# Optimization experiments

Measured on AMD Instinct MI355X. Metric: run time of the kernel, lower is better.

## Reference

```python
import jax, jax.numpy as jnp
import numpy as np

B, C, H, W = 8, 512, 64, 32
SE_MID = C // 16
BN_EPS = 1e-5


def conv1x1(x, w, b):
    # x: [B,Cin,H,W], w: [Cout,Cin], b: [Cout]
    return jnp.einsum('bchw,oc->bohw', x, w) + b[None, :, None, None]


def setup_inputs() -> dict:
    key = jax.random.key(0)
    ks = jax.random.split(key, 17)
    s = 0.05
    return {
        'x': jax.random.normal(ks[0], (B, C, H, W), jnp.float32),
        'g_w': jax.random.normal(ks[1], (1, C), jnp.float32) * s,
        'g_b': jax.random.normal(ks[2], (1,), jnp.float32) * s,
        'theta_w': jax.random.normal(ks[3], (1, C), jnp.float32) * s,
        'theta_b': jax.random.normal(ks[4], (1,), jnp.float32) * s,
        'phi_w': jax.random.normal(ks[5], (1, C), jnp.float32) * s,
        'phi_b': jax.random.normal(ks[6], (1,), jnp.float32) * s,
        'W_w': jax.random.normal(ks[7], (C, 1), jnp.float32) * s,
        'W_b': jax.random.normal(ks[8], (C,), jnp.float32) * s,
        'bn_gamma': jax.random.normal(ks[9], (C,), jnp.float32) * s + 1.0,
        'bn_beta': jax.random.normal(ks[10], (C,), jnp.float32) * s,
        'bn_mean': jax.random.normal(ks[11], (C,), jnp.float32) * s,
        'bn_var': jax.random.uniform(ks[12], (C,), jnp.float32, 0.5, 1.5),
        'se1_w': jax.random.normal(ks[13], (SE_MID, C), jnp.float32) * s,
        'se1_b': jnp.zeros((SE_MID,), jnp.float32),
        'se2_w': jax.random.normal(ks[14], (C, SE_MID), jnp.float32) * s,
        'se2_b': jnp.zeros((C,), jnp.float32),
    }


def reference(x, g_w, g_b, theta_w, theta_b, phi_w, phi_b, W_w, W_b,
              bn_gamma, bn_beta, bn_mean, bn_var, se1_w, se1_b, se2_w, se2_b):
    b, c, h, w = x.shape
    N = h * w
    # SE channel gate from global average pool: [B,C,1,1]
    x_avg = jnp.mean(x, axis=(2, 3), keepdims=True)
    se_mid = jax.nn.relu(conv1x1(x_avg, se1_w, se1_b))
    W_cw = jax.nn.sigmoid(conv1x1(se_mid, se2_w, se2_b))  # [B,C,1,1]

    # inter_channels == 1: each projection is a length-N vector per sample
    g_x = conv1x1(x, g_w, g_b).reshape(b, N)          # [B,N]
    theta_x = conv1x1(x, theta_w, theta_b).reshape(b, N)  # [B,N]
    phi_x = conv1x1(x, phi_w, phi_b).reshape(b, N)        # [B,N]

    # f[b,i,j] = theta[b,i] * phi[b,j]; row softmax over j; y = f_div_C @ g
    f = theta_x[:, :, None] * phi_x[:, None, :]       # [B,N,N]
    f_div_C = jax.nn.softmax(f, axis=-1)
    y = jnp.einsum('bij,bj->bi', f_div_C, g_x)        # [B,N]
    y = y.reshape(b, 1, h, w)

    # W: 1x1 conv (1 -> C) + BatchNorm2d (inference form with running stats)
    W_y = conv1x1(y, W_w, W_b)                        # [B,C,H,W]
    inv = bn_gamma / jnp.sqrt(bn_var + BN_EPS)
    W_y = (W_y - bn_mean[None, :, None, None]) * inv[None, :, None, None] \
          + bn_beta[None, :, None, None]

    return W_cw * W_y + x
```

## Files before the change

kernel.cpp:

```cpp
#include <hip/hip_runtime.h>

#define BB 8
#define CC 512
#define NN 2048
#define SEM 32
#define BN_EPS 1e-5f

#define NCC 16
#define NCHUNK (CC / NCC)
#define PIX 1024

__global__ __launch_bounds__(256) void k1(const float* __restrict__ x,
    const float* __restrict__ gw, const float* __restrict__ tw, const float* __restrict__ pw,
    float* __restrict__ pp,
    float* __restrict__ avgp)
{
    int tid = threadIdx.x;
    int wave = tid >> 6, lane = tid & 63;
    int blk = blockIdx.x;
    int ic = blk & 1;
    int cc = (blk >> 1) & (NCHUNK - 1);
    int b  = blk >> 6;
    int c0 = cc * NCC;

    const float4* xp = reinterpret_cast<const float4*>(x)
                     + ((size_t)(b * CC + c0) * (NN / 4)) + ic * (PIX / 4);

    float4 ag = {0,0,0,0}, at_ = {0,0,0,0}, ap = {0,0,0,0};
    float s[NCC];

    #pragma unroll
    for (int c = 0; c < NCC; ++c) {
        float4 v = xp[(size_t)c * (NN / 4) + tid];
        float wgc = gw[c0 + c], wtc = tw[c0 + c], wpc = pw[c0 + c];
        ag.x = fmaf(wgc, v.x, ag.x); ag.y = fmaf(wgc, v.y, ag.y);
        ag.z = fmaf(wgc, v.z, ag.z); ag.w = fmaf(wgc, v.w, ag.w);
        at_.x = fmaf(wtc, v.x, at_.x); at_.y = fmaf(wtc, v.y, at_.y);
        at_.z = fmaf(wtc, v.z, at_.z); at_.w = fmaf(wtc, v.w, at_.w);
        ap.x = fmaf(wpc, v.x, ap.x); ap.y = fmaf(wpc, v.y, ap.y);
        ap.z = fmaf(wpc, v.z, ap.z); ap.w = fmaf(wpc, v.w, ap.w);
        s[c] = (v.x + v.y) + (v.z + v.w);
    }

    size_t base = (((size_t)b * 2 + ic) * NCHUNK + cc) * PIX + tid * 4;
    const size_t karr = (size_t)BB * 2 * NCHUNK * PIX;
    *reinterpret_cast<float4*>(pp + 0 * karr + base) = ag;
    *reinterpret_cast<float4*>(pp + 1 * karr + base) = at_;
    *reinterpret_cast<float4*>(pp + 2 * karr + base) = ap;

    #pragma unroll
    for (int o = 32; o > 0; o >>= 1) {
        #pragma unroll
        for (int c = 0; c < NCC; ++c)
            s[c] += __shfl_down(s[c], o);
    }
    if (lane == 0) {
        #pragma unroll
        for (int c = 0; c < NCC; ++c)
            avgp[(size_t)(b * CC + c0 + c) * 8 + ic * 4 + wave] = s[c];
    }
}

__global__ __launch_bounds__(256) void k2(
    const float* __restrict__ pp,
    const float* __restrict__ gb, const float* __restrict__ tb, const float* __restrict__ pb,
    float* __restrict__ gx, float* __restrict__ tx, float* __restrict__ px)
{
    int tid = threadIdx.x;
    int half = blockIdx.x & 1;
    int ic   = (blockIdx.x >> 1) & 1;
    int b    = blockIdx.x >> 2;
    int p    = half * 512 + tid * 2;
    size_t base = ((((size_t)b * 2 + ic) * NCHUNK) * PIX + p) / 2;
    const size_t karr2 = (size_t)BB * 2 * NCHUNK * PIX / 2;
    const float2* pp2 = reinterpret_cast<const float2*>(pp);
    float2 g = {0,0}, t = {0,0}, ph = {0,0};
    #pragma unroll 8
    for (int cc = 0; cc < NCHUNK; ++cc) {
        float2 a = pp2[0 * karr2 + base + cc * (PIX / 2)];
        float2 c = pp2[1 * karr2 + base + cc * (PIX / 2)];
        float2 d = pp2[2 * karr2 + base + cc * (PIX / 2)];
        g.x += a.x;  g.y += a.y;
        t.x += c.x;  t.y += c.y;
        ph.x += d.x; ph.y += d.y;
    }
    int o = b * NN + ic * PIX + p;
    float gbv = gb[0], tbv = tb[0], pbv = pb[0];
    *reinterpret_cast<float2*>(gx + o) = make_float2(g.x + gbv, g.y + gbv);
    *reinterpret_cast<float2*>(tx + o) = make_float2(t.x + tbv, t.y + tbv);
    *reinterpret_cast<float2*>(px + o) = make_float2(ph.x + pbv, ph.y + pbv);
}

__global__ __launch_bounds__(256) void k3(
    const float* __restrict__ gx, const float* __restrict__ tx,
    const float* __restrict__ px, const float* __restrict__ avgp,
    const float* __restrict__ se1w, const float* __restrict__ se1b,
    const float* __restrict__ se2w, const float* __restrict__ se2b,
    const float* __restrict__ Ww, const float* __restrict__ Wb,
    const float* __restrict__ gamma, const float* __restrict__ beta,
    const float* __restrict__ mean, const float* __restrict__ var,
    float* __restrict__ y, float* __restrict__ Ac, float* __restrict__ Dc)
{
    int tid = threadIdx.x;

    if (blockIdx.x >= 1024) {
        int b = blockIdx.x - 1024;
        __shared__ float sA[CC];
        __shared__ float sP[SEM][8];
        __shared__ float sM[SEM];
        for (int c = tid; c < CC; c += 256) {
            const float* apt = avgp + (size_t)(b * CC + c) * 8;
            float s = 0.f;
            #pragma unroll
            for (int k = 0; k < 8; ++k) s += apt[k];
            sA[c] = s * (1.0f / NN);
        }
        __syncthreads();
        {
            int m = tid >> 3, sub = tid & 7;
            const float* w1 = se1w + m * CC + sub * 64;
            const float* a1 = sA + sub * 64;
            float s = 0.f;
            #pragma unroll
            for (int k = 0; k < 64; ++k) s = fmaf(a1[k], w1[k], s);
            sP[m][sub] = s;
        }
        __syncthreads();
        if (tid < SEM) {
            float t = 0.f;
            #pragma unroll
            for (int k = 0; k < 8; ++k) t += sP[tid][k];
            sM[tid] = fmaxf(t + se1b[tid], 0.f);
        }
        __syncthreads();
        for (int c = tid; c < CC; c += 256) {
            float s2 = 0.f;
            #pragma unroll
            for (int m = 0; m < SEM; ++m) s2 = fmaf(sM[m], se2w[c * SEM + m], s2);
            s2 += se2b[c];
            float wcw = 1.f / (1.f + __expf(-s2));
            float inv = gamma[c] * rsqrtf(var[c] + BN_EPS);
            Ac[b * CC + c] = wcw * Ww[c] * inv;
            Dc[b * CC + c] = wcw * ((Wb[c] - mean[c]) * inv + beta[c]);
        }
        return;
    }

    __shared__ float2 pg[NN];
    int b  = blockIdx.x >> 7;
    int i0 = (blockIdx.x & 127) << 4;
    for (int j = tid; j < NN; j += 256)
        pg[j] = make_float2(px[b * NN + j], gx[b * NN + j]);
    __syncthreads();

    int wave = tid >> 6, lane = tid & 63;
    int r0 = i0 + wave * 4;
    float t0 = tx[b * NN + r0 + 0];
    float t1 = tx[b * NN + r0 + 1];
    float t2 = tx[b * NN + r0 + 2];
    float t3 = tx[b * NN + r0 + 3];
    float s0 = 0.f, g0 = 0.f, s1 = 0.f, g1 = 0.f;
    float s2 = 0.f, g2 = 0.f, s3 = 0.f, g3 = 0.f;
    #pragma unroll 4
    for (int j = lane; j < NN; j += 64) {
        float2 v = pg[j];
        float e0 = __expf(fminf(t0 * v.x, 80.f));
        float e1 = __expf(fminf(t1 * v.x, 80.f));
        float e2 = __expf(fminf(t2 * v.x, 80.f));
        float e3 = __expf(fminf(t3 * v.x, 80.f));
        s0 += e0; g0 = fmaf(e0, v.y, g0);
        s1 += e1; g1 = fmaf(e1, v.y, g1);
        s2 += e2; g2 = fmaf(e2, v.y, g2);
        s3 += e3; g3 = fmaf(e3, v.y, g3);
    }
    for (int o = 32; o > 0; o >>= 1) {
        s0 += __shfl_down(s0, o); g0 += __shfl_down(g0, o);
        s1 += __shfl_down(s1, o); g1 += __shfl_down(g1, o);
        s2 += __shfl_down(s2, o); g2 += __shfl_down(g2, o);
        s3 += __shfl_down(s3, o); g3 += __shfl_down(g3, o);
    }
    if (lane == 0) {
        y[b * NN + r0 + 0] = g0 / s0;
        y[b * NN + r0 + 1] = g1 / s1;
        y[b * NN + r0 + 2] = g2 / s2;
        y[b * NN + r0 + 3] = g3 / s3;
    }
}

__global__ __launch_bounds__(256) void k4(
    const float* __restrict__ x, const float* __restrict__ y,
    const float* __restrict__ Ac, const float* __restrict__ Dc,
    float* __restrict__ out)
{
    int bc = blockIdx.x;
    int b = bc >> 9;
    float a = Ac[bc], d = Dc[bc];
    const float4* x4 = reinterpret_cast<const float4*>(x) + (size_t)bc * (NN / 4);
    const float4* y4 = reinterpret_cast<const float4*>(y) + (size_t)b * (NN / 4);
    float4* o4 = reinterpret_cast<float4*>(out) + (size_t)bc * (NN / 4);
    int tid = threadIdx.x;
    #pragma unroll
    for (int k = 0; k < 2; ++k) {
        int idx = k * 256 + tid;
        float4 xv = x4[idx], yv = y4[idx], ov;
        ov.x = fmaf(a, yv.x, d) + xv.x;
        ov.y = fmaf(a, yv.y, d) + xv.y;
        ov.z = fmaf(a, yv.z, d) + xv.z;
        ov.w = fmaf(a, yv.w, d) + xv.w;
        o4[idx] = ov;
    }
}

extern "C" void kernel_launch(void* const* d_in, const int* in_sizes, int n_in,
                              void* d_out, int out_size, void* d_ws, size_t ws_size,
                              hipStream_t stream) {
    const float* x    = (const float*)d_in[0];
    const float* gw   = (const float*)d_in[1];
    const float* gb   = (const float*)d_in[2];
    const float* tw   = (const float*)d_in[3];
    const float* tb   = (const float*)d_in[4];
    const float* pw   = (const float*)d_in[5];
    const float* pb   = (const float*)d_in[6];
    const float* Ww   = (const float*)d_in[7];
    const float* Wb   = (const float*)d_in[8];
    const float* gam  = (const float*)d_in[9];
    const float* bet  = (const float*)d_in[10];
    const float* mu   = (const float*)d_in[11];
    const float* var  = (const float*)d_in[12];
    const float* se1w = (const float*)d_in[13];
    const float* se1b = (const float*)d_in[14];
    const float* se2w = (const float*)d_in[15];
    const float* se2b = (const float*)d_in[16];

    float* ws   = (float*)d_ws;
    float* pp   = ws; ws += 3 * BB * 2 * NCHUNK * PIX;
    float* avgp = ws; ws += BB * CC * 8;
    float* gx   = ws; ws += BB * NN;
    float* tx   = ws; ws += BB * NN;
    float* px   = ws; ws += BB * NN;
    float* y    = ws; ws += BB * NN;
    float* Ac   = ws; ws += BB * CC;
    float* Dc   = ws; ws += BB * CC;
    float* out  = (float*)d_out;

    k1<<<BB * NCHUNK * 2, 256, 0, stream>>>(x, gw, tw, pw, pp, avgp);
    k2<<<BB * 2 * 2, 256, 0, stream>>>(pp, gb, tb, pb, gx, tx, px);
    k3<<<1024 + BB, 256, 0, stream>>>(gx, tx, px, avgp, se1w, se1b, se2w, se2b,
                                      Ww, Wb, gam, bet, mu, var, y, Ac, Dc);
    k4<<<BB * CC, 256, 0, stream>>>(x, y, Ac, Dc, out);
}
```

Baseline: 39.19 us.

## Fuse four kernels into one cooperative kernel with grid-wide syncs

Replaces the four separate launches with a single cooperative kernel of 256 blocks × 1024 threads, separated by grid.sync() between phases, with a multi-launch fallback if the cooperative launch fails. It also reshapes the per-phase work (full-row chunks in phase 1, 1024-thread reductions in phase 2, 16 channel rows per block in phase 4) and folds the g bias into Dc. The aim is to remove launch gaps and tail effects between the small kernels. In exchange it adds grid barrier cost and occupies only 256 blocks, which may underuse the GPU in the memory-bound phases.

After: 133.0 us. 3.39x slower.

```diff
diff --git a/kernel.cpp b/kernel.cpp
--- a/kernel.cpp
+++ b/kernel.cpp
@@ -1,164 +1,149 @@
 #include <hip/hip_runtime.h>
+#include <hip/hip_cooperative_groups.h>
+
+namespace cg = cooperative_groups;
 
 #define BB 8
 #define CC 512
 #define NN 2048
 #define SEM 32
 #define BN_EPS 1e-5f
-
 #define NCC 16
-#define NCHUNK (CC / NCC)
-#define PIX 1024
-
-__global__ __launch_bounds__(256) void k1(const float* __restrict__ x,
-    const float* __restrict__ gw, const float* __restrict__ tw, const float* __restrict__ pw,
-    float* __restrict__ pp,
-    float* __restrict__ avgp)
-{
-    int tid = threadIdx.x;
-    int wave = tid >> 6, lane = tid & 63;
-    int blk = blockIdx.x;
-    int ic = blk & 1;
-    int cc = (blk >> 1) & (NCHUNK - 1);
-    int b  = blk >> 6;
-    int c0 = cc * NCC;
-
-    const float4* xp = reinterpret_cast<const float4*>(x)
-                     + ((size_t)(b * CC + c0) * (NN / 4)) + ic * (PIX / 4);
-
-    float4 ag = {0,0,0,0}, at_ = {0,0,0,0}, ap = {0,0,0,0};
+#define NCHUNK 32
+#define KARR (BB * NCHUNK * NN)
+
+struct Ptrs {
+    const float *x, *gw, *tw, *pw, *gb, *tb, *pb;
+    const float *se1w, *se1b, *se2w, *se2b, *Ww, *Wb, *gam, *bet, *mu, *var;
+    float *pp, *avgp, *gx, *tx, *px, *y, *Ac, *Dc, *out;
+};
+
+__device__ __forceinline__ void phase1(const Ptrs& p, int blk, int tid) {
+    int b = blk >> 5, cc = blk & 31, c0 = cc * NCC;
+    const float2* xp2 = reinterpret_cast<const float2*>(p.x)
+                      + (size_t)(b * CC + c0) * (NN / 2) + tid;
+    float2 v[NCC];
+    #pragma unroll
+    for (int c = 0; c < NCC; ++c) v[c] = xp2[c * (NN / 2)];
+
+    float2 ag = {0,0}, at_ = {0,0}, ap = {0,0};
     float s[NCC];
-
     #pragma unroll
     for (int c = 0; c < NCC; ++c) {
-        float4 v = xp[(size_t)c * (NN / 4) + tid];
-        float wgc = gw[c0 + c], wtc = tw[c0 + c], wpc = pw[c0 + c];
-        ag.x = fmaf(wgc, v.x, ag.x); ag.y = fmaf(wgc, v.y, ag.y);
-        ag.z = fmaf(wgc, v.z, ag.z); ag.w = fmaf(wgc, v.w, ag.w);
-        at_.x = fmaf(wtc, v.x, at_.x); at_.y = fmaf(wtc, v.y, at_.y);
-        at_.z = fmaf(wtc, v.z, at_.z); at_.w = fmaf(wtc, v.w, at_.w);
-        ap.x = fmaf(wpc, v.x, ap.x); ap.y = fmaf(wpc, v.y, ap.y);
-        ap.z = fmaf(wpc, v.z, ap.z); ap.w = fmaf(wpc, v.w, ap.w);
-        s[c] = (v.x + v.y) + (v.z + v.w);
-    }
-
-    size_t base = (((size_t)b * 2 + ic) * NCHUNK + cc) * PIX + tid * 4;
-    const size_t karr = (size_t)BB * 2 * NCHUNK * PIX;
-    *reinterpret_cast<float4*>(pp + 0 * karr + base) = ag;
-    *reinterpret_cast<float4*>(pp + 1 * karr + base) = at_;
-    *reinterpret_cast<float4*>(pp + 2 * karr + base) = ap;
+        float wg = p.gw[c0 + c], wt = p.tw[c0 + c], wp = p.pw[c0 + c];
+        ag.x  = fmaf(wg, v[c].x, ag.x);  ag.y  = fmaf(wg, v[c].y, ag.y);
+        at_.x = fmaf(wt, v[c].x, at_.x); at_.y = fmaf(wt, v[c].y, at_.y);
+        ap.x  = fmaf(wp, v[c].x, ap.x);  ap.y  = fmaf(wp, v[c].y, ap.y);
+        s[c] = v[c].x + v[c].y;
+    }
+
+    size_t base = (size_t)blk * (NN / 2) + tid;
+    reinterpret_cast<float2*>(p.pp)[base] = ag;
+    reinterpret_cast<float2*>(p.pp + KARR)[base] = at_;
+    reinterpret_cast<float2*>(p.pp + 2 * (size_t)KARR)[base] = ap;
 
     #pragma unroll
     for (int o = 32; o > 0; o >>= 1) {
         #pragma unroll
-        for (int c = 0; c < NCC; ++c)
-            s[c] += __shfl_down(s[c], o);
-    }
+        for (int c = 0; c < NCC; ++c) s[c] += __shfl_down(s[c], o);
+    }
+    int wave = tid >> 6, lane = tid & 63;
     if (lane == 0) {
         #pragma unroll
         for (int c = 0; c < NCC; ++c)
-            avgp[(size_t)(b * CC + c0 + c) * 8 + ic * 4 + wave] = s[c];
-    }
-}
-
-__global__ __launch_bounds__(256) void k2(
-    const float* __restrict__ pp,
-    const float* __restrict__ gb, const float* __restrict__ tb, const float* __restrict__ pb,
-    float* __restrict__ gx, float* __restrict__ tx, float* __restrict__ px)
-{
-    int tid = threadIdx.x;
-    int half = blockIdx.x & 1;
-    int ic   = (blockIdx.x >> 1) & 1;
-    int b    = blockIdx.x >> 2;
-    int p    = half * 512 + tid * 2;
-    size_t base = ((((size_t)b * 2 + ic) * NCHUNK) * PIX + p) / 2;
-    const size_t karr2 = (size_t)BB * 2 * NCHUNK * PIX / 2;
-    const float2* pp2 = reinterpret_cast<const float2*>(pp);
-    float2 g = {0,0}, t = {0,0}, ph = {0,0};
-    #pragma unroll 8
-    for (int cc = 0; cc < NCHUNK; ++cc) {
-        float2 a = pp2[0 * karr2 + base + cc * (PIX / 2)];
-        float2 c = pp2[1 * karr2 + base + cc * (PIX / 2)];
-        float2 d = pp2[2 * karr2 + base + cc * (PIX / 2)];
-        g.x += a.x;  g.y += a.y;
-        t.x += c.x;  t.y += c.y;
-        ph.x += d.x; ph.y += d.y;
-    }
-    int o = b * NN + ic * PIX + p;
-    float gbv = gb[0], tbv = tb[0], pbv = pb[0];
-    *reinterpret_cast<float2*>(gx + o) = make_float2(g.x + gbv, g.y + gbv);
-    *reinterpret_cast<float2*>(tx + o) = make_float2(t.x + tbv, t.y + tbv);
-    *reinterpret_cast<float2*>(px + o) = make_float2(ph.x + pbv, ph.y + pbv);
-}
-
-__global__ __launch_bounds__(256) void k3(
-    const float* __restrict__ gx, const float* __restrict__ tx,
-    const float* __restrict__ px, const float* __restrict__ avgp,
-    const float* __restrict__ se1w, const float* __restrict__ se1b,
-    const float* __restrict__ se2w, const float* __restrict__ se2b,
-    const float* __restrict__ Ww, const float* __restrict__ Wb,
-    const float* __restrict__ gamma, const float* __restrict__ beta,
-    const float* __restrict__ mean, const float* __restrict__ var,
-    float* __restrict__ y, float* __restrict__ Ac, float* __restrict__ Dc)
-{
-    int tid = threadIdx.x;
-
-    if (blockIdx.x >= 1024) {
-        int b = blockIdx.x - 1024;
-        __shared__ float sA[CC];
-        __shared__ float sP[SEM][8];
-        __shared__ float sM[SEM];
-        for (int c = tid; c < CC; c += 256) {
-            const float* apt = avgp + (size_t)(b * CC + c) * 8;
-            float s = 0.f;
-            #pragma unroll
-            for (int k = 0; k < 8; ++k) s += apt[k];
-            sA[c] = s * (1.0f / NN);
-        }
-        __syncthreads();
-        {
-            int m = tid >> 3, sub = tid & 7;
-            const float* w1 = se1w + m * CC + sub * 64;
-            const float* a1 = sA + sub * 64;
-            float s = 0.f;
-            #pragma unroll
-            for (int k = 0; k < 64; ++k) s = fmaf(a1[k], w1[k], s);
-            sP[m][sub] = s;
+            p.avgp[(size_t)(b * CC + c0 + c) * 16 + wave] = s[c];
+    }
+}
+
+__device__ __forceinline__ void phase2(const Ptrs& p, int blk, int tid, float* smem) {
+    if (blk < 64) {
+        int b = blk >> 3, oct = blk & 7;
+        int pxi = tid & 255, rep = tid >> 8;
+        int pix = oct * 256 + pxi;
+        const float* base0 = p.pp + (size_t)b * NCHUNK * NN + pix + (size_t)rep * 8 * NN;
+        float a0 = 0.f, a1 = 0.f, a2 = 0.f;
+        #pragma unroll
+        for (int c = 0; c < 8; ++c) {
+            a0 += base0[(size_t)c * NN];
+            a1 += base0[(size_t)c * NN + KARR];
+            a2 += base0[(size_t)c * NN + 2 * (size_t)KARR];
+        }
+        smem[rep * 256 + pxi]        = a0;
+        smem[1024 + rep * 256 + pxi] = a1;
+        smem[2048 + rep * 256 + pxi] = a2;
+        __syncthreads();
+        if (tid < 768) {
+            int k = tid >> 8, px2 = tid & 255;
+            float* sk = smem + k * 1024;
+            float v = sk[px2] + sk[256 + px2] + sk[512 + px2] + sk[768 + px2];
+            int o = b * NN + oct * 256 + px2;
+            if (k == 0)      p.gx[o] = v;
+            else if (k == 1) p.tx[o] = v + p.tb[0];
+            else             p.px[o] = v + p.pb[0];
+        }
+    } else if (blk < 72) {
+        int b = blk - 64;
+        float* sA = smem;
+        float* sP = smem + 512;
+        float* sM = smem + 1024;
+        if (tid < 512) {
+            const float* apt = p.avgp + (size_t)(b * CC + tid) * 16;
+            float ssum = 0.f;
+            #pragma unroll
+            for (int k = 0; k < 16; ++k) ssum += apt[k];
+            sA[tid] = ssum * (1.0f / NN);
+        }
+        __syncthreads();
+        if (tid < 512) {
+            int m = tid >> 4, sub = tid & 15;
+            const float* w1 = p.se1w + m * CC + sub * 32;
+            const float* a1 = sA + sub * 32;
+            float ssum = 0.f;
+            #pragma unroll
+            for (int k = 0; k < 32; ++k) ssum = fmaf(a1[k], w1[k], ssum);
+            sP[m * 16 + sub] = ssum;
         }
         __syncthreads();
         if (tid < SEM) {
             float t = 0.f;
             #pragma unroll
-            for (int k = 0; k < 8; ++k) t += sP[tid][k];
-            sM[tid] = fmaxf(t + se1b[tid], 0.f);
-        }
-        __syncthreads();
-        for (int c = tid; c < CC; c += 256) {
+            for (int k = 0; k < 16; ++k) t += sP[tid * 16 + k];
+            sM[tid] = fmaxf(t + p.se1b[tid], 0.f);
+        }
+        __syncthreads();
+        if (tid < 512) {
+            int c = tid;
             float s2 = 0.f;
             #pragma unroll
-            for (int m = 0; m < SEM; ++m) s2 = fmaf(sM[m], se2w[c * SEM + m], s2);
-            s2 += se2b[c];
+            for (int m = 0; m < SEM; ++m) s2 = fmaf(sM[m], p.se2w[c * SEM + m], s2);
+            s2 += p.se2b[c];
             float wcw = 1.f / (1.f + __expf(-s2));
-            float inv = gamma[c] * rsqrtf(var[c] + BN_EPS);
-            Ac[b * CC + c] = wcw * Ww[c] * inv;
-            Dc[b * CC + c] = wcw * ((Wb[c] - mean[c]) * inv + beta[c]);
-        }
-        return;
-    }
-
-    __shared__ float2 pg[NN];
-    int b  = blockIdx.x >> 7;
-    int i0 = (blockIdx.x & 127) << 4;
-    for (int j = tid; j < NN; j += 256)
-        pg[j] = make_float2(px[b * NN + j], gx[b * NN + j]);
+            float inv = p.gam[c] * rsqrtf(p.var[c] + BN_EPS);
+            float A = wcw * p.Ww[c] * inv;
+            p.Ac[b * CC + c] = A;
+            p.Dc[b * CC + c] = wcw * ((p.Wb[c] - p.mu[c]) * inv + p.bet[c]) + A * p.gb[0];
+        }
+    }
+}
+
+__device__ __forceinline__ void phase3(const Ptrs& p, int blk, int tid, float* smem) {
+    float2* pg = reinterpret_cast<float2*>(smem);
+    int b = blk >> 5, rg = blk & 31;
+    const float* pxr = p.px + b * NN;
+    const float* gxr = p.gx + b * NN;
+    #pragma unroll
+    for (int j0 = 0; j0 < 2; ++j0) {
+        int j = j0 * 1024 + tid;
+        pg[j] = make_float2(pxr[j], gxr[j]);
+    }
     __syncthreads();
 
     int wave = tid >> 6, lane = tid & 63;
-    int r0 = i0 + wave * 4;
-    float t0 = tx[b * NN + r0 + 0];
-    float t1 = tx[b * NN + r0 + 1];
-    float t2 = tx[b * NN + r0 + 2];
-    float t3 = tx[b * NN + r0 + 3];
+    int r0 = rg * 64 + wave * 4;
+    float t0 = p.tx[b * NN + r0 + 0];
+    float t1 = p.tx[b * NN + r0 + 1];
+    float t2 = p.tx[b * NN + r0 + 2];
+    float t3 = p.tx[b * NN + r0 + 3];
     float s0 = 0.f, g0 = 0.f, s1 = 0.f, g1 = 0.f;
     float s2 = 0.f, g2 = 0.f, s3 = 0.f, g3 = 0.f;
     #pragma unroll 4
@@ -180,72 +165,104 @@
         s3 += __shfl_down(s3, o); g3 += __shfl_down(g3, o);
     }
     if (lane == 0) {
-        y[b * NN + r0 + 0] = g0 / s0;
-        y[b * NN + r0 + 1] = g1 / s1;
-        y[b * NN + r0 + 2] = g2 / s2;
-        y[b * NN + r0 + 3] = g3 / s3;
-    }
-}
-
-__global__ __launch_bounds__(256) void k4(
-    const float* __restrict__ x, const float* __restrict__ y,
-    const float* __restrict__ Ac, const float* __restrict__ Dc,
-    float* __restrict__ out)
-{
-    int bc = blockIdx.x;
-    int b = bc >> 9;
-    float a = Ac[bc], d = Dc[bc];
-    const float4* x4 = reinterpret_cast<const float4*>(x) + (size_t)bc * (NN / 4);
-    const float4* y4 = reinterpret_cast<const float4*>(y) + (size_t)b * (NN / 4);
-    float4* o4 = reinterpret_cast<float4*>(out) + (size_t)bc * (NN / 4);
-    int tid = threadIdx.x;
-    #pragma unroll
-    for (int k = 0; k < 2; ++k) {
-        int idx = k * 256 + tid;
-        float4 xv = x4[idx], yv = y4[idx], ov;
-        ov.x = fmaf(a, yv.x, d) + xv.x;
-        ov.y = fmaf(a, yv.y, d) + xv.y;
-        ov.z = fmaf(a, yv.z, d) + xv.z;
-        ov.w = fmaf(a, yv.w, d) + xv.w;
-        o4[idx] = ov;
-    }
-}
+        p.y[b * NN + r0 + 0] = g0 / s0;
+        p.y[b * NN + r0 + 1] = g1 / s1;
+        p.y[b * NN + r0 + 2] = g2 / s2;
+        p.y[b * NN + r0 + 3] = g3 / s3;
+    }
+}
+
+__device__ __forceinline__ void phase4(const Ptrs& p, int blk, int tid) {
+    int bc0 = blk * 16;
+    int b = blk >> 5;
+    int f4 = tid & 511, rr = tid >> 9;
+    float4 yv = reinterpret_cast<const float4*>(p.y + (size_t)b * NN)[f4];
+    float av[8], dv[8];
+    float4 xv[8];
+    #pragma unroll
+    for (int r = 0; r < 8; ++r) {
+        int bc = bc0 + rr * 8 + r;
+        av[r] = p.Ac[bc];
+        dv[r] = p.Dc[bc];
+        xv[r] = reinterpret_cast<const float4*>(p.x)[(size_t)bc * (NN / 4) + f4];
+    }
+    #pragma unroll
+    for (int r = 0; r < 8; ++r) {
+        int bc = bc0 + rr * 8 + r;
+        float4 ov;
+        ov.x = fmaf(av[r], yv.x, dv[r]) + xv[r].x;
+        ov.y = fmaf(av[r], yv.y, dv[r]) + xv[r].y;
+        ov.z = fmaf(av[r], yv.z, dv[r]) + xv[r].z;
+        ov.w = fmaf(av[r], yv.w, dv[r]) + xv[r].w;
+        reinterpret_cast<float4*>(p.out)[(size_t)bc * (NN / 4) + f4] = ov;
+    }
+}
+
+__global__ __launch_bounds__(1024, 4) void kcoop(Ptrs p) {
+    __shared__ float smem[4096];
+    cg::grid_group g = cg::this_grid();
+    int blk = blockIdx.x, tid = threadIdx.x;
+    phase1(p, blk, tid);
+    g.sync();
+    phase2(p, blk, tid, smem);
+    g.sync();
+    phase3(p, blk, tid, smem);
+    g.sync();
+    phase4(p, blk, tid);
+}
+
+__global__ __launch_bounds__(1024, 4) void fb1(Ptrs p) { phase1(p, blockIdx.x, threadIdx.x); }
+__global__ __launch_bounds__(1024, 4) void fb2(Ptrs p) {
+    __shared__ float smem[4096];
+    phase2(p, blockIdx.x, threadIdx.x, smem);
+}
+__global__ __launch_bounds__(1024, 4) void fb3(Ptrs p) {
+    __shared__ float smem[4096];
+    phase3(p, blockIdx.x, threadIdx.x, smem);
+}
+__global__ __launch_bounds__(1024, 4) void fb4(Ptrs p) { phase4(p, blockIdx.x, threadIdx.x); }
 
 extern "C" void kernel_launch(void* const* d_in, const int* in_sizes, int n_in,
                               void* d_out, int out_size, void* d_ws, size_t ws_size,
                               hipStream_t stream) {
-    const float* x    = (const float*)d_in[0];
-    const float* gw   = (const float*)d_in[1];
-    const float* gb   = (const float*)d_in[2];
-    const float* tw   = (const float*)d_in[3];
-    const float* tb   = (const float*)d_in[4];
-    const float* pw   = (const float*)d_in[5];
-    const float* pb   = (const float*)d_in[6];
-    const float* Ww   = (const float*)d_in[7];
-    const float* Wb   = (const float*)d_in[8];
-    const float* gam  = (const float*)d_in[9];
-    const float* bet  = (const float*)d_in[10];
-    const float* mu   = (const float*)d_in[11];
-    const float* var  = (const float*)d_in[12];
-    const float* se1w = (const float*)d_in[13];
-    const float* se1b = (const float*)d_in[14];
-    const float* se2w = (const float*)d_in[15];
-    const float* se2b = (const float*)d_in[16];
-
-    float* ws   = (float*)d_ws;
-    float* pp   = ws; ws += 3 * BB * 2 * NCHUNK * PIX;
-    float* avgp = ws; ws += BB * CC * 8;
-    float* gx   = ws; ws += BB * NN;
-    float* tx   = ws; ws += BB * NN;
-    float* px   = ws; ws += BB * NN;
-    float* y    = ws; ws += BB * NN;
-    float* Ac   = ws; ws += BB * CC;
-    float* Dc   = ws; ws += BB * CC;
-    float* out  = (float*)d_out;
-
-    k1<<<BB * NCHUNK * 2, 256, 0, stream>>>(x, gw, tw, pw, pp, avgp);
-    k2<<<BB * 2 * 2, 256, 0, stream>>>(pp, gb, tb, pb, gx, tx, px);
-    k3<<<1024 + BB, 256, 0, stream>>>(gx, tx, px, avgp, se1w, se1b, se2w, se2b,
-                                      Ww, Wb, gam, bet, mu, var, y, Ac, Dc);
-    k4<<<BB * CC, 256, 0, stream>>>(x, y, Ac, Dc, out);
-}
+    Ptrs P;
+    P.x    = (const float*)d_in[0];
+    P.gw   = (const float*)d_in[1];
+    P.gb   = (const float*)d_in[2];
+    P.tw   = (const float*)d_in[3];
+    P.tb   = (const float*)d_in[4];
+    P.pw   = (const float*)d_in[5];
+    P.pb   = (const float*)d_in[6];
+    P.Ww   = (const float*)d_in[7];
+    P.Wb   = (const float*)d_in[8];
+    P.gam  = (const float*)d_in[9];
+    P.bet  = (const float*)d_in[10];
+    P.mu   = (const float*)d_in[11];
+    P.var  = (const float*)d_in[12];
+    P.se1w = (const float*)d_in[13];
+    P.se1b = (const float*)d_in[14];
+    P.se2w = (const float*)d_in[15];
+    P.se2b = (const float*)d_in[16];
+
+    float* ws = (float*)d_ws;
+    P.pp   = ws; ws += 3 * (size_t)KARR;
+    P.avgp = ws; ws += BB * CC * 16;
+    P.gx   = ws; ws += BB * NN;
+    P.tx   = ws; ws += BB * NN;
+    P.px   = ws; ws += BB * NN;
+    P.y    = ws; ws += BB * NN;
+    P.Ac   = ws; ws += BB * CC;
+    P.Dc   = ws; ws += BB * CC;
+    P.out  = (float*)d_out;
+
+    void* args[] = { (void*)&P };
+    hipError_t err = hipLaunchCooperativeKernel(reinterpret_cast<void*>(kcoop),
+                                                dim3(256), dim3(1024), args, 0, stream);
+    if (err != hipSuccess) {
+        (void)hipGetLastError();
+        fb1<<<256, 1024, 0, stream>>>(P);
+        fb2<<<72,  1024, 0, stream>>>(P);
+        fb3<<<256, 1024, 0, stream>>>(P);
+        fb4<<<256, 1024, 0, stream>>>(P);
+    }
+}
```

## Rebalance projection partial sums, widen k2 grid, use exp2 in attention loop

Applied to the files above, without the earlier changes.

The first kernel now processes 32-channel groups with float2 loads over two pixel halves, halving the partial-sum array. The reduction kernel gets a wider grid (192 blocks, one output array each) instead of 32 blocks. The g bias is folded into the per-channel D constant, so g is stored without bias. The attention loop uses exp2 with a prescaled theta and processes two columns per iteration from separate shared arrays. This aims to cut partial-sum traffic, improve parallelism in the reduction stage, and reduce per-element exp cost. The trade-off is fewer, heavier k1 blocks and a changed exponent clamp.

New measurement: 43.92 us. +12.1%, slower.

```diff
diff --git a/kernel.cpp b/kernel.cpp
--- a/kernel.cpp
+++ b/kernel.cpp
@@ -5,95 +5,92 @@
 #define NN 2048
 #define SEM 32
 #define BN_EPS 1e-5f
-
-#define NCC 16
-#define NCHUNK (CC / NCC)
-#define PIX 1024
+#define LOG2E 1.4426950408889634f
+
+#define CG 32
+#define NG (CC / CG)
+#define KARR (NG * BB * NN)
 
 __global__ __launch_bounds__(256) void k1(const float* __restrict__ x,
     const float* __restrict__ gw, const float* __restrict__ tw, const float* __restrict__ pw,
-    float* __restrict__ pp,
-    float* __restrict__ avgp)
+    float* __restrict__ pp, float* __restrict__ avgp)
 {
     int tid = threadIdx.x;
     int wave = tid >> 6, lane = tid & 63;
     int blk = blockIdx.x;
-    int ic = blk & 1;
-    int cc = (blk >> 1) & (NCHUNK - 1);
-    int b  = blk >> 6;
-    int c0 = cc * NCC;
-
-    const float4* xp = reinterpret_cast<const float4*>(x)
-                     + ((size_t)(b * CC + c0) * (NN / 4)) + ic * (PIX / 4);
-
-    float4 ag = {0,0,0,0}, at_ = {0,0,0,0}, ap = {0,0,0,0};
-    float s[NCC];
-
-    #pragma unroll
-    for (int c = 0; c < NCC; ++c) {
-        float4 v = xp[(size_t)c * (NN / 4) + tid];
-        float wgc = gw[c0 + c], wtc = tw[c0 + c], wpc = pw[c0 + c];
-        ag.x = fmaf(wgc, v.x, ag.x); ag.y = fmaf(wgc, v.y, ag.y);
-        ag.z = fmaf(wgc, v.z, ag.z); ag.w = fmaf(wgc, v.w, ag.w);
-        at_.x = fmaf(wtc, v.x, at_.x); at_.y = fmaf(wtc, v.y, at_.y);
-        at_.z = fmaf(wtc, v.z, at_.z); at_.w = fmaf(wtc, v.w, at_.w);
-        ap.x = fmaf(wpc, v.x, ap.x); ap.y = fmaf(wpc, v.y, ap.y);
-        ap.z = fmaf(wpc, v.z, ap.z); ap.w = fmaf(wpc, v.w, ap.w);
-        s[c] = (v.x + v.y) + (v.z + v.w);
-    }
-
-    size_t base = (((size_t)b * 2 + ic) * NCHUNK + cc) * PIX + tid * 4;
-    const size_t karr = (size_t)BB * 2 * NCHUNK * PIX;
-    *reinterpret_cast<float4*>(pp + 0 * karr + base) = ag;
-    *reinterpret_cast<float4*>(pp + 1 * karr + base) = at_;
-    *reinterpret_cast<float4*>(pp + 2 * karr + base) = ap;
+    int h = blk & 1;
+    int g = (blk >> 1) & (NG - 1);
+    int b = blk >> 5;
+    int c0 = g * CG;
+
+    const float2* xp = reinterpret_cast<const float2*>(x)
+                     + (size_t)(b * CC + c0) * (NN / 2) + h * 512 + tid;
+
+    float2 ag0 = {0,0}, at0 = {0,0}, ap0 = {0,0};
+    float2 ag1 = {0,0}, at1 = {0,0}, ap1 = {0,0};
+    float s[CG];
+
+    #pragma unroll 8
+    for (int c = 0; c < CG; ++c) {
+        float2 v0 = xp[(size_t)c * (NN / 2)];
+        float2 v1 = xp[(size_t)c * (NN / 2) + 256];
+        float wg = gw[c0 + c], wt = tw[c0 + c], wp = pw[c0 + c];
+        ag0.x = fmaf(wg, v0.x, ag0.x); ag0.y = fmaf(wg, v0.y, ag0.y);
+        at0.x = fmaf(wt, v0.x, at0.x); at0.y = fmaf(wt, v0.y, at0.y);
+        ap0.x = fmaf(wp, v0.x, ap0.x); ap0.y = fmaf(wp, v0.y, ap0.y);
+        ag1.x = fmaf(wg, v1.x, ag1.x); ag1.y = fmaf(wg, v1.y, ag1.y);
+        at1.x = fmaf(wt, v1.x, at1.x); at1.y = fmaf(wt, v1.y, at1.y);
+        ap1.x = fmaf(wp, v1.x, ap1.x); ap1.y = fmaf(wp, v1.y, ap1.y);
+        s[c] = (v0.x + v0.y) + (v1.x + v1.y);
+    }
+
+    size_t i0 = (size_t)(g * BB + b) * 1024 + h * 512 + tid;
+    float2* pp2 = reinterpret_cast<float2*>(pp);
+    pp2[i0]                  = ag0;
+    pp2[i0 + 256]            = ag1;
+    pp2[KARR / 2 + i0]       = at0;
+    pp2[KARR / 2 + i0 + 256] = at1;
+    pp2[KARR + i0]           = ap0;
+    pp2[KARR + i0 + 256]     = ap1;
 
     #pragma unroll
     for (int o = 32; o > 0; o >>= 1) {
         #pragma unroll
-        for (int c = 0; c < NCC; ++c)
-            s[c] += __shfl_down(s[c], o);
+        for (int c = 0; c < CG; ++c) s[c] += __shfl_down(s[c], o);
     }
     if (lane == 0) {
         #pragma unroll
-        for (int c = 0; c < NCC; ++c)
-            avgp[(size_t)(b * CC + c0 + c) * 8 + ic * 4 + wave] = s[c];
+        for (int c = 0; c < CG; ++c)
+            avgp[(size_t)(b * CC + c0 + c) * 8 + h * 4 + wave] = s[c];
     }
 }
 
 __global__ __launch_bounds__(256) void k2(
     const float* __restrict__ pp,
-    const float* __restrict__ gb, const float* __restrict__ tb, const float* __restrict__ pb,
+    const float* __restrict__ tb, const float* __restrict__ pb,
     float* __restrict__ gx, float* __restrict__ tx, float* __restrict__ px)
 {
     int tid = threadIdx.x;
-    int half = blockIdx.x & 1;
-    int ic   = (blockIdx.x >> 1) & 1;
-    int b    = blockIdx.x >> 2;
-    int p    = half * 512 + tid * 2;
-    size_t base = ((((size_t)b * 2 + ic) * NCHUNK) * PIX + p) / 2;
-    const size_t karr2 = (size_t)BB * 2 * NCHUNK * PIX / 2;
-    const float2* pp2 = reinterpret_cast<const float2*>(pp);
-    float2 g = {0,0}, t = {0,0}, ph = {0,0};
-    #pragma unroll 8
-    for (int cc = 0; cc < NCHUNK; ++cc) {
-        float2 a = pp2[0 * karr2 + base + cc * (PIX / 2)];
-        float2 c = pp2[1 * karr2 + base + cc * (PIX / 2)];
-        float2 d = pp2[2 * karr2 + base + cc * (PIX / 2)];
-        g.x += a.x;  g.y += a.y;
-        t.x += c.x;  t.y += c.y;
-        ph.x += d.x; ph.y += d.y;
-    }
-    int o = b * NN + ic * PIX + p;
-    float gbv = gb[0], tbv = tb[0], pbv = pb[0];
-    *reinterpret_cast<float2*>(gx + o) = make_float2(g.x + gbv, g.y + gbv);
-    *reinterpret_cast<float2*>(tx + o) = make_float2(t.x + tbv, t.y + tbv);
-    *reinterpret_cast<float2*>(px + o) = make_float2(ph.x + pbv, ph.y + pbv);
+    int oct = blockIdx.x & 7;
+    int g3  = blockIdx.x >> 3;
+    int k   = g3 % 3;
+    int b   = g3 / 3;
+    int p   = oct * 256 + tid;
+    const float* base = pp + (size_t)k * KARR + (size_t)b * NN + p;
+    float v = 0.f;
+    #pragma unroll
+    for (int g = 0; g < NG; ++g)
+        v += base[(size_t)g * BB * NN];
+    int o = b * NN + p;
+    if (k == 0)      gx[o] = v;
+    else if (k == 1) tx[o] = v + tb[0];
+    else             px[o] = v + pb[0];
 }
 
 __global__ __launch_bounds__(256) void k3(
     const float* __restrict__ gx, const float* __restrict__ tx,
     const float* __restrict__ px, const float* __restrict__ avgp,
+    const float* __restrict__ gb,
     const float* __restrict__ se1w, const float* __restrict__ se1b,
     const float* __restrict__ se2w, const float* __restrict__ se2b,
     const float* __restrict__ Ww, const float* __restrict__ Wb,
@@ -101,38 +98,40 @@
     const float* __restrict__ mean, const float* __restrict__ var,
     float* __restrict__ y, float* __restrict__ Ac, float* __restrict__ Dc)
 {
+    __shared__ float smem[4096];
     int tid = threadIdx.x;
 
     if (blockIdx.x >= 1024) {
         int b = blockIdx.x - 1024;
-        __shared__ float sA[CC];
-        __shared__ float sP[SEM][8];
-        __shared__ float sM[SEM];
+        float* sA = smem;
+        float* sP = smem + 512;
+        float* sM = smem + 768;
         for (int c = tid; c < CC; c += 256) {
             const float* apt = avgp + (size_t)(b * CC + c) * 8;
-            float s = 0.f;
-            #pragma unroll
-            for (int k = 0; k < 8; ++k) s += apt[k];
-            sA[c] = s * (1.0f / NN);
+            float ssum = 0.f;
+            #pragma unroll
+            for (int k = 0; k < 8; ++k) ssum += apt[k];
+            sA[c] = ssum * (1.0f / NN);
         }
         __syncthreads();
         {
             int m = tid >> 3, sub = tid & 7;
             const float* w1 = se1w + m * CC + sub * 64;
             const float* a1 = sA + sub * 64;
-            float s = 0.f;
-            #pragma unroll
-            for (int k = 0; k < 64; ++k) s = fmaf(a1[k], w1[k], s);
-            sP[m][sub] = s;
+            float ssum = 0.f;
+            #pragma unroll
+            for (int k = 0; k < 64; ++k) ssum = fmaf(a1[k], w1[k], ssum);
+            sP[m * 8 + sub] = ssum;
         }
         __syncthreads();
         if (tid < SEM) {
             float t = 0.f;
             #pragma unroll
-            for (int k = 0; k < 8; ++k) t += sP[tid][k];
+            for (int k = 0; k < 8; ++k) t += sP[tid * 8 + k];
             sM[tid] = fmaxf(t + se1b[tid], 0.f);
         }
         __syncthreads();
+        float gbv = gb[0];
         for (int c = tid; c < CC; c += 256) {
             float s2 = 0.f;
             #pragma unroll
@@ -140,38 +139,54 @@
             s2 += se2b[c];
             float wcw = 1.f / (1.f + __expf(-s2));
             float inv = gamma[c] * rsqrtf(var[c] + BN_EPS);
-            Ac[b * CC + c] = wcw * Ww[c] * inv;
-            Dc[b * CC + c] = wcw * ((Wb[c] - mean[c]) * inv + beta[c]);
+            float A = wcw * Ww[c] * inv;
+            Ac[b * CC + c] = A;
+            Dc[b * CC + c] = wcw * ((Wb[c] - mean[c]) * inv + beta[c]) + A * gbv;
         }
         return;
     }
 
-    __shared__ float2 pg[NN];
+    float* spx = smem;
+    float* sgx = smem + 2048;
     int b  = blockIdx.x >> 7;
     int i0 = (blockIdx.x & 127) << 4;
-    for (int j = tid; j < NN; j += 256)
-        pg[j] = make_float2(px[b * NN + j], gx[b * NN + j]);
+    {
+        const float4* pxr = reinterpret_cast<const float4*>(px + (size_t)b * NN);
+        const float4* gxr = reinterpret_cast<const float4*>(gx + (size_t)b * NN);
+        float4* spx4 = reinterpret_cast<float4*>(spx);
+        float4* sgx4 = reinterpret_cast<float4*>(sgx);
+        #pragma unroll
+        for (int w = 0; w < 2; ++w) {
+            int idx = w * 256 + tid;
+            spx4[idx] = pxr[idx];
+            sgx4[idx] = gxr[idx];
+        }
+    }
     __syncthreads();
 
     int wave = tid >> 6, lane = tid & 63;
     int r0 = i0 + wave * 4;
-    float t0 = tx[b * NN + r0 + 0];
-    float t1 = tx[b * NN + r0 + 1];
-    float t2 = tx[b * NN + r0 + 2];
-    float t3 = tx[b * NN + r0 + 3];
+    float t0 = tx[b * NN + r0 + 0] * LOG2E;
+    float t1 = tx[b * NN + r0 + 1] * LOG2E;
+    float t2 = tx[b * NN + r0 + 2] * LOG2E;
+    float t3 = tx[b * NN + r0 + 3] * LOG2E;
     float s0 = 0.f, g0 = 0.f, s1 = 0.f, g1 = 0.f;
     float s2 = 0.f, g2 = 0.f, s3 = 0.f, g3 = 0.f;
+    const float2* spx2 = reinterpret_cast<const float2*>(spx);
+    const float2* sgx2 = reinterpret_cast<const float2*>(sgx);
     #pragma unroll 4
-    for (int j = lane; j < NN; j += 64) {
-        float2 v = pg[j];
-        float e0 = __expf(fminf(t0 * v.x, 80.f));
-        float e1 = __expf(fminf(t1 * v.x, 80.f));
-        float e2 = __expf(fminf(t2 * v.x, 80.f));
-        float e3 = __expf(fminf(t3 * v.x, 80.f));
-        s0 += e0; g0 = fmaf(e0, v.y, g0);
-        s1 += e1; g1 = fmaf(e1, v.y, g1);
-        s2 += e2; g2 = fmaf(e2, v.y, g2);
-        s3 += e3; g3 = fmaf(e3, v.y, g3);
+    for (int it = 0; it < 16; ++it) {
+        int jj = it * 64 + lane;
+        float2 xv = spx2[jj];
+        float2 gv = sgx2[jj];
+        float e0a = exp2f(fminf(t0 * xv.x, 115.f)), e0b = exp2f(fminf(t0 * xv.y, 115.f));
+        float e1a = exp2f(fminf(t1 * xv.x, 115.f)), e1b = exp2f(fminf(t1 * xv.y, 115.f));
+        float e2a = exp2f(fminf(t2 * xv.x, 115.f)), e2b = exp2f(fminf(t2 * xv.y, 115.f));
+        float e3a = exp2f(fminf(t3 * xv.x, 115.f)), e3b = exp2f(fminf(t3 * xv.y, 115.f));
+        s0 += e0a + e0b; g0 = fmaf(e0a, gv.x, fmaf(e0b, gv.y, g0));
+        s1 += e1a + e1b; g1 = fmaf(e1a, gv.x, fmaf(e1b, gv.y, g1));
+        s2 += e2a + e2b; g2 = fmaf(e2a, gv.x, fmaf(e2b, gv.y, g2));
+        s3 += e3a + e3b; g3 = fmaf(e3a, gv.x, fmaf(e3b, gv.y, g3));
     }
     for (int o = 32; o > 0; o >>= 1) {
         s0 += __shfl_down(s0, o); g0 += __shfl_down(g0, o);
@@ -233,7 +248,7 @@
     const float* se2b = (const float*)d_in[16];
 
     float* ws   = (float*)d_ws;
-    float* pp   = ws; ws += 3 * BB * 2 * NCHUNK * PIX;
+    float* pp   = ws; ws += 3 * (size_t)KARR;
     float* avgp = ws; ws += BB * CC * 8;
     float* gx   = ws; ws += BB * NN;
     float* tx   = ws; ws += BB * NN;
@@ -243,9 +258,9 @@
     float* Dc   = ws; ws += BB * CC;
     float* out  = (float*)d_out;
 
-    k1<<<BB * NCHUNK * 2, 256, 0, stream>>>(x, gw, tw, pw, pp, avgp);
-    k2<<<BB * 2 * 2, 256, 0, stream>>>(pp, gb, tb, pb, gx, tx, px);
-    k3<<<1024 + BB, 256, 0, stream>>>(gx, tx, px, avgp, se1w, se1b, se2w, se2b,
+    k1<<<BB * NG * 2, 256, 0, stream>>>(x, gw, tw, pw, pp, avgp);
+    k2<<<BB * 3 * 8, 256, 0, stream>>>(pp, tb, pb, gx, tx, px);
+    k3<<<1024 + BB, 256, 0, stream>>>(gx, tx, px, avgp, gb, se1w, se1b, se2w, se2b,
                                       Ww, Wb, gam, bet, mu, var, y, Ac, Dc);
     k4<<<BB * CC, 256, 0, stream>>>(x, y, Ac, Dc, out);
 }
```
